# Performance work log

Measured on AMD Instinct MI355X. Metric: run time of the kernel, lower is better.

The kernel has to match this reference:

```python
import jax, jax.numpy as jnp
import numpy as np

DIM = 128
SCALE = (DIM // 8) ** -0.5  # head_dim**-0.5 with default num_heads=8 (heads never actually split)


def _attention(x, fm, qw, kw, vw, pw, pb):
    # x, fm: [B, C, H, W]
    B, C, H, W = x.shape
    xt = x.reshape(B, C, H * W).transpose(0, 2, 1)   # [B, N, C]
    ft = fm.reshape(B, C, H * W).transpose(0, 2, 1)  # [B, N, C]
    q = jnp.einsum('bnc,dc->bnd', xt, qw)
    k = jnp.einsum('bnc,dc->bnd', ft, kw)
    v = jnp.einsum('bnc,dc->bnd', xt, vw)
    attn = jax.nn.softmax(jnp.einsum('bnd,bmd->bnm', q, k) * SCALE, axis=-1)
    o = jnp.einsum('bnm,bmd->bnd', attn, v)
    o = jnp.einsum('bnd,ed->bne', o, pw) + pb
    return o.transpose(0, 2, 1).reshape(B, C, H, W)


def setup_inputs() -> dict:
    key = jax.random.key(0)
    ks = jax.random.split(key, 16)
    B, C, H, W = 1, DIM, 96, 96
    s = 0.02
    inp = {
        'x': jax.random.normal(ks[0], (B, C, H, W), jnp.float32),
        'featuremap': jax.random.normal(ks[1], (B, C, H, W), jnp.float32),
        'hm': jax.random.uniform(ks[2], (B, 1, H, W), jnp.float32),
        'obj_qw': jax.random.normal(ks[3], (C, C), jnp.float32) * s,
        'obj_kw': jax.random.normal(ks[4], (C, C), jnp.float32) * s,
        'obj_vw': jax.random.normal(ks[5], (C, C), jnp.float32) * s,
        'obj_pw': jax.random.normal(ks[6], (C, C), jnp.float32) * s,
        'obj_pb': jnp.zeros((C,), jnp.float32),
        'bg_qw': jax.random.normal(ks[7], (C, C), jnp.float32) * s,
        'bg_kw': jax.random.normal(ks[8], (C, C), jnp.float32) * s,
        'bg_vw': jax.random.normal(ks[9], (C, C), jnp.float32) * s,
        'bg_pw': jax.random.normal(ks[10], (C, C), jnp.float32) * s,
        'bg_pb': jnp.zeros((C,), jnp.float32),
        'conv_w': jax.random.normal(ks[11], (C, C, 3, 3), jnp.float32) * s,
        'conv_b': jnp.zeros((C,), jnp.float32),
    }
    return inp


def reference(x, featuremap, hm, obj_qw, obj_kw, obj_vw, obj_pw, obj_pb,
              bg_qw, bg_kw, bg_vw, bg_pw, bg_pb, conv_w, conv_b):
    obj_mask = jnp.where(hm > 0.3, 1.0, 0.01)
    bg_mask = jnp.where(hm <= 0.3, 1.0, 0.01)
    obj_att = _attention(x * obj_mask, featuremap * obj_mask,
                         obj_qw, obj_kw, obj_vw, obj_pw, obj_pb)
    bg_att = _attention(x * bg_mask, featuremap * bg_mask,
                        bg_qw, bg_kw, bg_vw, bg_pw, bg_pb)
    am = obj_att + bg_att
    out = jax.lax.conv_general_dilated(
        am, conv_w, window_strides=(1, 1), padding='SAME',
        dimension_numbers=('NCHW', 'OIHW', 'NCHW'))
    return out + conv_b[None, :, None, None]
```

## Files before the change

### kernel.cpp

```cpp
#include <hip/hip_runtime.h>


typedef unsigned short u16;
typedef short bf16x8 __attribute__((ext_vector_type(8)));
typedef float f32x4 __attribute__((ext_vector_type(4)));

#define MFMA(a, b, c) __builtin_amdgcn_mfma_f32_16x16x32_bf16((a), (b), (c), 0, 0, 0)

#define NN 9216
#define CC 128
#define SPLIT 8
#define FITERS 36

__device__ __forceinline__ u16 f2b(float f) {
  union { float f; unsigned int u; } v; v.f = f;
  unsigned int u = v.u + 0x7fffu + ((v.u >> 16) & 1u);
  return (u16)(u >> 16);
}

__device__ __forceinline__ unsigned int f2b2(float lo, float hi) {
  return (unsigned int)f2b(lo) | ((unsigned int)f2b(hi) << 16);
}

__device__ __forceinline__ unsigned int pkhi(float a, float b) {
  return __builtin_amdgcn_perm(__float_as_uint(b), __float_as_uint(a), 0x07060302u);
}

__device__ __forceinline__ bf16x8 ldb(const u16* p) { return *(const bf16x8*)p; }

__device__ __forceinline__ void ldsdma16(const void* g, void* l) {
  __builtin_amdgcn_global_load_lds(
      (const __attribute__((address_space(1))) unsigned int*)g,
      (__attribute__((address_space(3))) unsigned int*)l, 16, 0, 0);
}

__global__ void k_prep(const float* __restrict__ x, const float* __restrict__ fm,
                       const float* qw0, const float* kw0, const float* vw0,
                       const float* pw0, const float* qw1, const float* kw1,
                       const float* vw1, const float* pw1,
                       const float* __restrict__ cw,
                       u16* __restrict__ xt, u16* __restrict__ fmt,
                       u16* __restrict__ wall, u16* __restrict__ wp) {
  int bid = blockIdx.x, tid = threadIdx.x;
  if (bid < 2304) {
    __shared__ float tile[32][33];
    int z = bid / 1152, b2 = bid % 1152;
    const float* src = z ? fm : x;
    u16* dst = z ? fmt : xt;
    int n0 = (b2 % 288) * 32, c0 = (b2 / 288) * 32;
    int tx = tid & 31, ty = tid >> 5;
#pragma unroll
    for (int i = 0; i < 4; i++)
      tile[ty + i * 8][tx] = src[(c0 + ty + i * 8) * NN + n0 + tx];
    __syncthreads();
#pragma unroll
    for (int i = 0; i < 4; i++)
      dst[(n0 + ty + i * 8) * CC + c0 + tx] = f2b(tile[tx][ty + i * 8]);
  } else if (bid < 2816) {
    const float* arr[8] = {qw0, kw0, vw0, pw0, qw1, kw1, vw1, pw1};
    int b2 = bid - 2304;
    int a = b2 >> 6;
    int i = (b2 & 63) * 256 + tid;
    wall[a * 16384 + i] = f2b(arr[a][i]);
  } else {
    int i = (bid - 2816) * 256 + tid;
    int khkw = i >> 14; int rem = i & 16383; int o = rem >> 7; int ii = rem & 127;
    wp[i] = f2b(cw[(o * 128 + ii) * 9 + khkw]);
  }
}

__global__ __launch_bounds__(256) void k_qkv(
    const u16* __restrict__ xt, const u16* __restrict__ fmt, const float* __restrict__ hm,
    const u16* __restrict__ wall, u16* __restrict__ Q, u16* __restrict__ K,
    u16* __restrict__ Vt) {
  __shared__ __align__(16) u16 sst[8192];
  int tid = threadIdx.x;
  int wid = tid >> 6, lane = tid & 63;
  int quad = lane >> 4, c = lane & 15;
  int nb64 = blockIdx.x * 64;
  int nb = nb64 + wid * 16;
  int arr = blockIdx.y;
  int attn = arr / 3, kind = arr % 3;
  const u16* A = (kind == 1) ? fmt : xt;
  const u16* W = wall + (attn * 4 + kind) * 16384;

  bf16x8 wf[2][4];
#pragma unroll
  for (int k4 = 0; k4 < 4; k4++)
    wf[0][k4] = ldb(W + c * CC + k4 * 32 + quad * 8);

  if (kind < 2) {
    bf16x8 af[4];
#pragma unroll
    for (int k4 = 0; k4 < 4; k4++)
      af[k4] = ldb(A + (nb + c) * CC + k4 * 32 + quad * 8);
    float msk[4];
#pragma unroll
    for (int r = 0; r < 4; r++) {
      bool obj = hm[nb + quad * 4 + r] > 0.3f;
      float mv = (attn == 0) ? (obj ? 1.f : 0.01f) : (obj ? 0.01f : 1.f);
      msk[r] = (kind == 0) ? mv * 0.3606737602222409f : mv;
    }
    u16* tw = sst + wid * 2048;
#pragma unroll
    for (int dt = 0; dt < 8; dt++) {
      int cur = dt & 1;
      if (dt < 7) {
#pragma unroll
        for (int k4 = 0; k4 < 4; k4++)
          wf[cur ^ 1][k4] = ldb(W + ((dt + 1) * 16 + c) * CC + k4 * 32 + quad * 8);
      }
      f32x4 acc = {0.f, 0.f, 0.f, 0.f};
#pragma unroll
      for (int k4 = 0; k4 < 4; k4++)
        acc = MFMA(af[k4], wf[cur][k4], acc);
#pragma unroll
      for (int r = 0; r < 4; r++)
        tw[(quad * 4 + r) * 128 + dt * 16 + c] = f2b(acc[r] * msk[r]);
    }
    u16* out = (kind == 0 ? Q : K) + attn * NN * CC + nb * CC;
#pragma unroll
    for (int i = 0; i < 4; i++) {
      uint4 v = *(const uint4*)((const char*)tw + i * 1024 + lane * 16);
      *(uint4*)((char*)out + i * 1024 + lane * 16) = v;
    }
  } else {
    bf16x8 bfr[4];
#pragma unroll
    for (int k4 = 0; k4 < 4; k4++)
      bfr[k4] = ldb(A + (nb + c) * CC + k4 * 32 + quad * 8);
    bool obj = hm[nb + c] > 0.3f;
    float mv = (attn == 0) ? (obj ? 1.f : 0.01f) : (obj ? 0.01f : 1.f);
#pragma unroll
    for (int dt = 0; dt < 8; dt++) {
      int cur = dt & 1;
      if (dt < 7) {
#pragma unroll
        for (int k4 = 0; k4 < 4; k4++)
          wf[cur ^ 1][k4] = ldb(W + ((dt + 1) * 16 + c) * CC + k4 * 32 + quad * 8);
      }
      f32x4 acc = {0.f, 0.f, 0.f, 0.f};
#pragma unroll
      for (int k4 = 0; k4 < 4; k4++)
        acc = MFMA(wf[cur][k4], bfr[k4], acc);
#pragma unroll
      for (int r = 0; r < 4; r++)
        sst[(dt * 16 + quad * 4 + r) * 64 + wid * 16 + c] = f2b(acc[r] * mv);
    }
    __syncthreads();
    char* vt0 = (char*)(Vt + attn * CC * NN) + nb64 * 2;
#pragma unroll
    for (int i = 0; i < 4; i++) {
      int idx = wid * 4 + i;
      int drow = idx * 8 + (lane >> 3);
      int ch = lane & 7;
      uint4 v = *(const uint4*)((const char*)sst + drow * 128 + ch * 16);
      *(uint4*)(vt0 + (long)drow * (NN * 2) + ch * 16) = v;
    }
  }
}

__global__ __launch_bounds__(256, 2) void k_flash(
    const u16* __restrict__ Q, const u16* __restrict__ K, const u16* __restrict__ Vt,
    u16* __restrict__ U, float* __restrict__ L) {
  __shared__ __align__(16) char lds[47104];
  int tid = threadIdx.x;
  int wid = tid >> 6, lane = tid & 63;
  int quad = lane >> 4, c = lane & 15;
  int b = blockIdx.x;
  int qg = b >> 4; int combo = b & 15;
  int attn = combo >> 3; int ks = combo & 7;
  int nb = qg * 128 + wid * 32;
  const u16* q = Q + attn * NN * CC;
  const u16* kg = K + attn * NN * CC;
  const u16* vg = Vt + attn * CC * NN;
  int kb0 = ks * 1152;

  int srow = tid >> 4;
  int chn = (tid & 15) ^ (srow & 7);
  const u16* gkp0 = kg + (kb0 + srow) * CC + chn * 8;
  const u16* gkp1 = gkp0 + 16 * CC;
  int vrow = tid >> 2, vqd = tid & 3;
  const u16* gvp0 = vg + vrow * NN + kb0 + vqd * 8;
  const u16* gvp1 = gvp0 + 64 * NN;
  int lv0 = vrow * 80 + vqd * 16, lv1 = lv0 + 64 * 80;

  bf16x8 qf[2][4];
#pragma unroll
  for (int qt = 0; qt < 2; qt++)
#pragma unroll
    for (int k4 = 0; k4 < 4; k4++)
      qf[qt][k4] = ldb(q + (nb + qt * 16 + c) * CC + k4 * 32 + quad * 8);

  const bf16x8 ONES = {(short)0x3F80, (short)0x3F80, (short)0x3F80, (short)0x3F80,
                       (short)0x3F80, (short)0x3F80, (short)0x3F80, (short)0x3F80};

  f32x4 O[2][8];
  f32x4 lacc[2];
#pragma unroll
  for (int qt = 0; qt < 2; qt++) {
#pragma unroll
    for (int dt = 0; dt < 8; dt++) O[qt][dt] = (f32x4){0.f, 0.f, 0.f, 0.f};
    lacc[qt] = (f32x4){0.f, 0.f, 0.f, 0.f};
  }

  char* Pw = lds + 36864 + wid * 2560;

  ldsdma16(gkp0, lds + wid * 1024);
  ldsdma16(gkp1, lds + 4096 + wid * 1024);
  uint4 gv0 = *(const uint4*)gvp0, gv1 = *(const uint4*)gvp1;

  for (int it = 0; it < FITERS; it++) {
    char* kb_lds = lds + ((it & 1) ? 8192 : 0);
    char* vb_lds = lds + 16384 + ((it & 1) ? 10240 : 0);
    *(uint4*)(vb_lds + lv0) = gv0;
    *(uint4*)(vb_lds + lv1) = gv1;
    __syncthreads();
    if (it + 1 < FITERS) {
      char* kn = lds + (((it + 1) & 1) ? 8192 : 0);
      gkp0 += 32 * CC; gkp1 += 32 * CC;
      ldsdma16(gkp0, kn + wid * 1024);
      ldsdma16(gkp1, kn + 4096 + wid * 1024);
      gvp0 += 32; gvp1 += 32;
      gv0 = *(const uint4*)gvp0; gv1 = *(const uint4*)gvp1;
    }

#pragma unroll
    for (int kt = 0; kt < 2; kt++) {
      bf16x8 kf[4];
#pragma unroll
      for (int k4 = 0; k4 < 4; k4++)
        kf[k4] = *(const bf16x8*)(kb_lds + (kt * 16 + c) * 256 +
                                  (((k4 * 4 + quad) ^ (c & 7)) * 16));
#pragma unroll
      for (int qt = 0; qt < 2; qt++) {
        f32x4 s = {0.f, 0.f, 0.f, 0.f};
#pragma unroll
        for (int k4 = 0; k4 < 4; k4++) s = MFMA(kf[k4], qf[qt][k4], s);
        uint2 d;
        d.x = pkhi(__builtin_amdgcn_exp2f(s[0]), __builtin_amdgcn_exp2f(s[1]));
        d.y = pkhi(__builtin_amdgcn_exp2f(s[2]), __builtin_amdgcn_exp2f(s[3]));
        *(uint2*)(Pw + (qt * 16 + c) * 80 + kt * 32 + quad * 8) = d;
      }
    }

    bf16x8 pf[2];
#pragma unroll
    for (int qt = 0; qt < 2; qt++) {
      pf[qt] = *(const bf16x8*)(Pw + (qt * 16 + c) * 80 + quad * 16);
      lacc[qt] = MFMA(pf[qt], ONES, lacc[qt]);
    }
#pragma unroll
    for (int dt = 0; dt < 8; dt++) {
      bf16x8 vf = *(const bf16x8*)(vb_lds + (dt * 16 + c) * 80 + quad * 16);
#pragma unroll
      for (int qt = 0; qt < 2; qt++) O[qt][dt] = MFMA(pf[qt], vf, O[qt][dt]);
    }
  }

  int p = attn * SPLIT + ks;
  u16* up = U + (long)(p * NN + nb) * CC;
#pragma unroll
  for (int qt = 0; qt < 2; qt++)
#pragma unroll
    for (int dt = 0; dt < 8; dt++)
#pragma unroll
      for (int r = 0; r < 4; r++)
        up[(qt * 16 + quad * 4 + r) * CC + dt * 16 + c] = f2b(O[qt][dt][r]);
  if (c == 0) {
#pragma unroll
    for (int qt = 0; qt < 2; qt++)
#pragma unroll
      for (int r = 0; r < 4; r++)
        L[p * NN + nb + qt * 16 + quad * 4 + r] = lacc[qt][r];
  }
}

__global__ __launch_bounds__(256) void k_pm(const u16* __restrict__ U,
                                            const float* __restrict__ L,
                                            const u16* __restrict__ wall,
                                            const float* __restrict__ pb0,
                                            const float* __restrict__ pb1,
                                            u16* __restrict__ amt) {
  __shared__ __align__(16) char omt[8704];
  __shared__ float linv[32];
  int tid = threadIdx.x;
  int nb = blockIdx.x * 16;

  {
    if (tid < 32) {
      int a = tid >> 4, r = tid & 15;
      float l = 0.f;
#pragma unroll
      for (int s = 0; s < SPLIT; s++) l += L[(a * SPLIT + s) * NN + nb + r];
      linv[tid] = 1.f / l;
    }
    int a = tid >> 7, rr = (tid >> 3) & 15, dg = tid & 7;
    uint4 ua[SPLIT], ub[SPLIT];
#pragma unroll
    for (int s = 0; s < SPLIT; s++) {
      const u16* src = U + (long)((a * SPLIT + s) * NN + nb + rr) * CC + dg * 16;
      ua[s] = *(const uint4*)src;
      ub[s] = *(const uint4*)(src + 8);
    }
    float acc[16];
#pragma unroll
    for (int j = 0; j < 16; j++) acc[j] = 0.f;
#pragma unroll
    for (int s = 0; s < SPLIT; s++) {
      const unsigned int* w0 = (const unsigned int*)&ua[s];
      const unsigned int* w1 = (const unsigned int*)&ub[s];
#pragma unroll
      for (int j = 0; j < 4; j++) {
        acc[j * 2 + 0] += __uint_as_float(w0[j] << 16);
        acc[j * 2 + 1] += __uint_as_float(w0[j] & 0xffff0000u);
        acc[8 + j * 2 + 0] += __uint_as_float(w1[j] << 16);
        acc[8 + j * 2 + 1] += __uint_as_float(w1[j] & 0xffff0000u);
      }
    }
    __syncthreads();
    float inv = linv[a * 16 + rr];
    unsigned int pk[8];
#pragma unroll
    for (int j = 0; j < 8; j++)
      pk[j] = f2b2(acc[j * 2] * inv, acc[j * 2 + 1] * inv);
    uint4* dst = (uint4*)(omt + (a * 16 + rr) * 272 + dg * 32);
    dst[0] = *(uint4*)&pk[0];
    dst[1] = *(uint4*)&pk[4];
  }
  __syncthreads();

  int wid = tid >> 6, lane = tid & 63;
  int quad = lane >> 4, c = lane & 15;
  bf16x8 af[2][4];
#pragma unroll
  for (int a = 0; a < 2; a++)
#pragma unroll
    for (int k4 = 0; k4 < 4; k4++)
      af[a][k4] = *(const bf16x8*)(omt + (a * 16 + c) * 272 + k4 * 64 + quad * 16);
  const u16* wpo = wall + 3 * 16384;
  const u16* wpb = wall + 7 * 16384;
  __syncthreads();
  u16* pmt = (u16*)omt;
#pragma unroll
  for (int eh = 0; eh < 2; eh++) {
    int et = wid * 2 + eh;
    f32x4 acc = {0.f, 0.f, 0.f, 0.f};
#pragma unroll
    for (int k4 = 0; k4 < 4; k4++)
      acc = MFMA(af[0][k4], ldb(wpo + (et * 16 + c) * CC + k4 * 32 + quad * 8), acc);
#pragma unroll
    for (int k4 = 0; k4 < 4; k4++)
      acc = MFMA(af[1][k4], ldb(wpb + (et * 16 + c) * CC + k4 * 32 + quad * 8), acc);
    float bias = pb0[et * 16 + c] + pb1[et * 16 + c];
#pragma unroll
    for (int r = 0; r < 4; r++)
      pmt[(quad * 4 + r) * 128 + et * 16 + c] = f2b(acc[r] + bias);
  }
  __syncthreads();
  uint4 v = *(const uint4*)((const char*)pmt + wid * 1024 + lane * 16);
  *(uint4*)((char*)(amt + nb * CC) + wid * 1024 + lane * 16) = v;
}

__global__ __launch_bounds__(256) void k_conv(const u16* __restrict__ amt,
                                              const u16* __restrict__ wp,
                                              const float* __restrict__ cb,
                                              float* __restrict__ out) {
  __shared__ __align__(16) char halo[54 * 272];
  int tid = threadIdx.x;
  int wid = tid >> 6, lane = tid & 63;
  int quad = lane >> 4, c = lane & 15;
  int p0 = blockIdx.x * 16;
  int h = p0 / 96, w0 = p0 % 96;

  for (int t = tid; t < 54 * 16; t += 256) {
    int hp = t >> 4, ch16 = t & 15;
    int hr = hp / 18, hc = hp % 18;
    int hh = h + hr - 1, ww = w0 + hc - 1;
    uint4 v = {0u, 0u, 0u, 0u};
    if (hh >= 0 && hh < 96 && ww >= 0 && ww < 96)
      v = *(const uint4*)(amt + (hh * 96 + ww) * CC + ch16 * 8);
    *(uint4*)(halo + hp * 272 + ch16 * 16) = v;
  }
  __syncthreads();

  int p = p0 + c;
  f32x4 acc0 = {0.f, 0.f, 0.f, 0.f};
  f32x4 acc1 = {0.f, 0.f, 0.f, 0.f};
  int ot0 = wid * 2, ot1 = wid * 2 + 1;

  bf16x8 wa[2][4], wb[2][4];
#define LOAD_W(BUF, T)                                                        \
  {                                                                           \
    const u16* wbase = wp + (T) * 16384;                                      \
    _Pragma("unroll") for (int k4 = 0; k4 < 4; k4++) {                        \
      wa[BUF][k4] = ldb(wbase + (ot0 * 16 + c) * CC + k4 * 32 + quad * 8);    \
      wb[BUF][k4] = ldb(wbase + (ot1 * 16 + c) * CC + k4 * 32 + quad * 8);    \
    }                                                                         \
  }

  LOAD_W(0, 0)
#pragma unroll
  for (int t = 0; t < 9; t++) {
    int cur = t & 1;
    if (t < 8) LOAD_W(cur ^ 1, t + 1)
    int kh = t / 3, kw = t % 3;
    const char* hrow = halo + (kh * 18 + kw + c) * 272;
#pragma unroll
    for (int k4 = 0; k4 < 4; k4++) {
      bf16x8 bv = *(const bf16x8*)(hrow + k4 * 64 + quad * 16);
      acc0 = MFMA(wa[cur][k4], bv, acc0);
      acc1 = MFMA(wb[cur][k4], bv, acc1);
    }
  }
#undef LOAD_W

#pragma unroll
  for (int r = 0; r < 4; r++) {
    int o0 = ot0 * 16 + quad * 4 + r;
    int o1 = ot1 * 16 + quad * 4 + r;
    out[o0 * NN + p] = acc0[r] + cb[o0];
    out[o1 * NN + p] = acc1[r] + cb[o1];
  }
}

extern "C" void kernel_launch(void* const* d_in, const int* in_sizes, int n_in,
                              void* d_out, int out_size, void* d_ws, size_t ws_size,
                              hipStream_t stream) {
  (void)in_sizes; (void)n_in; (void)out_size; (void)ws_size;
  const float* x   = (const float*)d_in[0];
  const float* fm  = (const float*)d_in[1];
  const float* hm  = (const float*)d_in[2];
  const float* qw0 = (const float*)d_in[3];
  const float* kw0 = (const float*)d_in[4];
  const float* vw0 = (const float*)d_in[5];
  const float* pw0 = (const float*)d_in[6];
  const float* pb0 = (const float*)d_in[7];
  const float* qw1 = (const float*)d_in[8];
  const float* kw1 = (const float*)d_in[9];
  const float* vw1 = (const float*)d_in[10];
  const float* pw1 = (const float*)d_in[11];
  const float* pb1 = (const float*)d_in[12];
  const float* cw  = (const float*)d_in[13];
  const float* cb  = (const float*)d_in[14];
  float* out = (float*)d_out;
  char* ws = (char*)d_ws;

  u16*   XT   = (u16*)(ws + 0);
  u16*   FMT  = (u16*)(ws + 2359296);
  u16*   WALL = (u16*)(ws + 4718592);
  u16*   WCV  = (u16*)(ws + 4980736);
  u16*   QQ   = (u16*)(ws + 5275648);
  u16*   KK   = (u16*)(ws + 9994240);
  u16*   VT   = (u16*)(ws + 14712832);
  u16*   UU   = (u16*)(ws + 19431424);
  float* LL   = (float*)(ws + 57180160);
  u16*   AMT  = KK;

  k_prep<<<3392, 256, 0, stream>>>(x, fm, qw0, kw0, vw0, pw0, qw1, kw1, vw1, pw1,
                                   cw, XT, FMT, WALL, WCV);
  k_qkv<<<dim3(144, 6), 256, 0, stream>>>(XT, FMT, hm, WALL, QQ, KK, VT);
  k_flash<<<1152, 256, 0, stream>>>(QQ, KK, VT, UU, LL);
  k_pm<<<576, 256, 0, stream>>>(UU, LL, WALL, pb0, pb1, AMT);
  k_conv<<<576, 256, 0, stream>>>(AMT, WCV, cb, out);
}
```

Measured before the change: 241.7 us.

## Fuse split-K merge and projection into flash kernel via last-block atomic counter

Removes the separate merge+projection kernel launch. Each flash block bumps a per-query-group atomic counter, and the last of the 16 split blocks combines the partial outputs and applies the output projection for its 128 rows. This saves a kernel launch and the gap between kernels. In exchange it adds a memset, threadfences, and a serialized tail in which a single block processes 128 rows, which lowers parallelism for the merge work. The AMT and counter buffers now reuse the XT/FMT workspace.

```diff
diff --git a/kernel.cpp b/kernel.cpp
--- a/kernel.cpp
+++ b/kernel.cpp
@@ -162,8 +162,11 @@
 
 __global__ __launch_bounds__(256, 2) void k_flash(
     const u16* __restrict__ Q, const u16* __restrict__ K, const u16* __restrict__ Vt,
-    u16* __restrict__ U, float* __restrict__ L) {
+    u16* __restrict__ U, float* __restrict__ L,
+    const u16* __restrict__ wall, const float* __restrict__ pb0,
+    const float* __restrict__ pb1, u16* __restrict__ amt, int* __restrict__ cnt) {
   __shared__ __align__(16) char lds[47104];
+  __shared__ int sdone;
   int tid = threadIdx.x;
   int wid = tid >> 6, lane = tid & 63;
   int quad = lane >> 4, c = lane & 15;
@@ -274,32 +277,33 @@
       for (int r = 0; r < 4; r++)
         L[p * NN + nb + qt * 16 + quad * 4 + r] = lacc[qt][r];
   }
-}
-
-__global__ __launch_bounds__(256) void k_pm(const u16* __restrict__ U,
-                                            const float* __restrict__ L,
-                                            const u16* __restrict__ wall,
-                                            const float* __restrict__ pb0,
-                                            const float* __restrict__ pb1,
-                                            u16* __restrict__ amt) {
-  __shared__ __align__(16) char omt[8704];
-  __shared__ float linv[32];
-  int tid = threadIdx.x;
-  int nb = blockIdx.x * 16;
-
-  {
+
+  __threadfence();
+  __syncthreads();
+  if (tid == 0) sdone = atomicAdd(&cnt[qg], 1);
+  __syncthreads();
+  if (sdone != 15) return;
+  __threadfence();
+
+  char* omt = lds;
+  float* linv = (float*)(lds + 8704);
+  const u16* wpo = wall + 3 * 16384;
+  const u16* wpb = wall + 7 * 16384;
+
+  for (int g = 0; g < 8; g++) {
+    int rb = qg * 128 + g * 16;
     if (tid < 32) {
       int a = tid >> 4, r = tid & 15;
       float l = 0.f;
 #pragma unroll
-      for (int s = 0; s < SPLIT; s++) l += L[(a * SPLIT + s) * NN + nb + r];
+      for (int s = 0; s < SPLIT; s++) l += L[(a * SPLIT + s) * NN + rb + r];
       linv[tid] = 1.f / l;
     }
     int a = tid >> 7, rr = (tid >> 3) & 15, dg = tid & 7;
     uint4 ua[SPLIT], ub[SPLIT];
 #pragma unroll
     for (int s = 0; s < SPLIT; s++) {
-      const u16* src = U + (long)((a * SPLIT + s) * NN + nb + rr) * CC + dg * 16;
+      const u16* src = U + (long)((a * SPLIT + s) * NN + rb + rr) * CC + dg * 16;
       ua[s] = *(const uint4*)src;
       ub[s] = *(const uint4*)(src + 8);
     }
@@ -320,46 +324,42 @@
     }
     __syncthreads();
     float inv = linv[a * 16 + rr];
-    unsigned int pk[8];
+    unsigned int pk2[8];
 #pragma unroll
     for (int j = 0; j < 8; j++)
-      pk[j] = f2b2(acc[j * 2] * inv, acc[j * 2 + 1] * inv);
+      pk2[j] = f2b2(acc[j * 2] * inv, acc[j * 2 + 1] * inv);
     uint4* dst = (uint4*)(omt + (a * 16 + rr) * 272 + dg * 32);
-    dst[0] = *(uint4*)&pk[0];
-    dst[1] = *(uint4*)&pk[4];
-  }
-  __syncthreads();
-
-  int wid = tid >> 6, lane = tid & 63;
-  int quad = lane >> 4, c = lane & 15;
-  bf16x8 af[2][4];
-#pragma unroll
-  for (int a = 0; a < 2; a++)
-#pragma unroll
-    for (int k4 = 0; k4 < 4; k4++)
-      af[a][k4] = *(const bf16x8*)(omt + (a * 16 + c) * 272 + k4 * 64 + quad * 16);
-  const u16* wpo = wall + 3 * 16384;
-  const u16* wpb = wall + 7 * 16384;
-  __syncthreads();
-  u16* pmt = (u16*)omt;
-#pragma unroll
-  for (int eh = 0; eh < 2; eh++) {
-    int et = wid * 2 + eh;
-    f32x4 acc = {0.f, 0.f, 0.f, 0.f};
-#pragma unroll
-    for (int k4 = 0; k4 < 4; k4++)
-      acc = MFMA(af[0][k4], ldb(wpo + (et * 16 + c) * CC + k4 * 32 + quad * 8), acc);
-#pragma unroll
-    for (int k4 = 0; k4 < 4; k4++)
-      acc = MFMA(af[1][k4], ldb(wpb + (et * 16 + c) * CC + k4 * 32 + quad * 8), acc);
-    float bias = pb0[et * 16 + c] + pb1[et * 16 + c];
-#pragma unroll
-    for (int r = 0; r < 4; r++)
-      pmt[(quad * 4 + r) * 128 + et * 16 + c] = f2b(acc[r] + bias);
-  }
-  __syncthreads();
-  uint4 v = *(const uint4*)((const char*)pmt + wid * 1024 + lane * 16);
-  *(uint4*)((char*)(amt + nb * CC) + wid * 1024 + lane * 16) = v;
+    dst[0] = *(uint4*)&pk2[0];
+    dst[1] = *(uint4*)&pk2[4];
+    __syncthreads();
+
+    bf16x8 af[2][4];
+#pragma unroll
+    for (int a2 = 0; a2 < 2; a2++)
+#pragma unroll
+      for (int k4 = 0; k4 < 4; k4++)
+        af[a2][k4] = *(const bf16x8*)(omt + (a2 * 16 + c) * 272 + k4 * 64 + quad * 16);
+    __syncthreads();
+    u16* pmt = (u16*)omt;
+#pragma unroll
+    for (int eh = 0; eh < 2; eh++) {
+      int et = wid * 2 + eh;
+      f32x4 pa = {0.f, 0.f, 0.f, 0.f};
+#pragma unroll
+      for (int k4 = 0; k4 < 4; k4++)
+        pa = MFMA(af[0][k4], ldb(wpo + (et * 16 + c) * CC + k4 * 32 + quad * 8), pa);
+#pragma unroll
+      for (int k4 = 0; k4 < 4; k4++)
+        pa = MFMA(af[1][k4], ldb(wpb + (et * 16 + c) * CC + k4 * 32 + quad * 8), pa);
+      float bias = pb0[et * 16 + c] + pb1[et * 16 + c];
+#pragma unroll
+      for (int r = 0; r < 4; r++)
+        pmt[(quad * 4 + r) * 128 + et * 16 + c] = f2b(pa[r] + bias);
+    }
+    __syncthreads();
+    uint4 v = *(const uint4*)((const char*)pmt + wid * 1024 + lane * 16);
+    *(uint4*)((char*)(amt + rb * CC) + wid * 1024 + lane * 16) = v;
+  }
 }
 
 __global__ __launch_bounds__(256) void k_conv(const u16* __restrict__ amt,
@@ -455,12 +455,13 @@
   u16*   VT   = (u16*)(ws + 14712832);
   u16*   UU   = (u16*)(ws + 19431424);
   float* LL   = (float*)(ws + 57180160);
-  u16*   AMT  = KK;
+  u16*   AMT  = XT;
+  int*   CNT  = (int*)FMT;
 
   k_prep<<<3392, 256, 0, stream>>>(x, fm, qw0, kw0, vw0, pw0, qw1, kw1, vw1, pw1,
                                    cw, XT, FMT, WALL, WCV);
   k_qkv<<<dim3(144, 6), 256, 0, stream>>>(XT, FMT, hm, WALL, QQ, KK, VT);
-  k_flash<<<1152, 256, 0, stream>>>(QQ, KK, VT, UU, LL);
-  k_pm<<<576, 256, 0, stream>>>(UU, LL, WALL, pb0, pb1, AMT);
+  hipMemsetAsync(CNT, 0, 72 * sizeof(int), stream);
+  k_flash<<<1152, 256, 0, stream>>>(QQ, KK, VT, UU, LL, WALL, pb0, pb1, AMT, CNT);
   k_conv<<<576, 256, 0, stream>>>(AMT, WCV, cb, out);
 }
```

Result: slower. 477.3 us (+97.4%).
